# Kernel tuning notes

Hardware: AMD Instinct MI355X
Metric: run time of the kernel (lower is better)

The kernel has to match this reference:

```python
import jax, jax.numpy as jnp
import numpy as np

EPS = 1e-12
TOPK = 6

def _l2norm(x):
    # matches torch F.normalize(p=2, eps=1e-12)
    n = jnp.linalg.norm(x, axis=-1, keepdims=True)
    return x / jnp.maximum(n, EPS)

def setup_inputs() -> dict:
    key = jax.random.key(0)
    k1, k2 = jax.random.split(key)
    nC, M, P, d = 5, 512, 196, 384
    support = jax.random.normal(k1, (nC, P, d), dtype=jnp.float32)
    query = jax.random.normal(k2, (M, P, d), dtype=jnp.float32)
    scale_cls = jnp.full((1,), 10.0, dtype=jnp.float32)  # init value in module
    bias = jnp.zeros((1,), dtype=jnp.float32)
    return {"support": support, "query": query, "scale_cls": scale_cls, "bias": bias}

def reference(support, query, scale_cls, bias):
    q = _l2norm(query)      # [M, P, d]
    s = _l2norm(support)    # [nC, P, d]
    # batched cosine similarity between every query patch and support patch
    sim = jnp.einsum('mpd,cqd->mcpq', q, s)   # [M, nC, P, P]
    # max over support patches, then sum of top-6 query-patch matches
    m = sim.max(axis=3)                        # [M, nC, P]
    top6 = jax.lax.top_k(m, TOPK)[0].sum(axis=-1)  # [M, nC]
    cls_scores = top6[None]                    # [1, M, nC] (unsqueeze(0))
    return scale_cls * (cls_scores + bias)
```

## Files before the change

### kernel.cpp

```cpp
#include <hip/hip_runtime.h>
#include <hip/hip_bf16.h>
#include <cstdint>

typedef __attribute__((ext_vector_type(8))) short short8;
typedef __attribute__((ext_vector_type(4))) float floatx4;

#define NC   5
#define PP   196
#define DD   384
#define MM   512
#define ROWS (MM * PP)
#define NRB  1568
#define BR   64
#define EPSN 1e-12f

#define NTILES      16
#define TILE_BYTES  49152
#define KSTEP_BYTES 4096

__device__ __forceinline__ unsigned enc_f(float f) {
    unsigned u = __float_as_uint(f);
    return (u & 0x80000000u) ? ~u : (u | 0x80000000u);
}
__device__ __forceinline__ float dec_f(unsigned u) {
    unsigned b = (u & 0x80000000u) ? (u ^ 0x80000000u) : ~u;
    return __uint_as_float(b);
}
#define ENC_NEG_INF 0x007FFFFFu

__device__ __forceinline__ int cls_of(int col) {
    return (col >= 784) ? 4 : (col >= 588) ? 3 : (col >= 392) ? 2 : (col >= 196) ? 1 : 0;
}

__global__ __launch_bounds__(256) void k_norm0(const float* __restrict__ sup,
                                               float* __restrict__ sinv) {
    int wid = threadIdx.x >> 6, lane = threadIdx.x & 63;
    int r = blockIdx.x * 4 + wid;
    if (r >= NC * PP) return;
    const float* src = sup + (size_t)r * DD;
    float s = 0.f;
    #pragma unroll
    for (int j = 0; j < 6; ++j) { float v = src[lane + j * 64]; s += v * v; }
    #pragma unroll
    for (int off = 1; off < 64; off <<= 1) s += __shfl_xor(s, off, 64);
    if (lane == 0) sinv[r] = 1.0f / fmaxf(sqrtf(s), EPSN);
}

__global__ __launch_bounds__(256) void k_swz(const float* __restrict__ sup,
                                             const float* __restrict__ sinv,
                                             __hip_bfloat16* __restrict__ snw) {
    int s = blockIdx.x * 256 + threadIdx.x;
    int lane = s & 63;
    int r1 = s >> 6;
    int ct = r1 & 3;
    int r2 = r1 >> 2;
    int kk = r2 % 12;
    int t  = r2 / 12;
    int c16 = lane & 15, quad = lane >> 4;
    int col = t * 64 + ct * 16 + c16;
    if (col > NC * PP - 1) col = NC * PP - 1;
    int srow = col;
    const float* sp = sup + (size_t)srow * DD + kk * 32 + quad * 8;
    float inv = sinv[srow];
    alignas(16) __hip_bfloat16 hb[8];
    #pragma unroll
    for (int e = 0; e < 8; ++e) hb[e] = __float2bfloat16(sp[e] * inv);
    *(uint4*)((char*)snw + (size_t)s * 16) = *(const uint4*)hb;
}

__global__ __launch_bounds__(256, 2) void k_gemm_max(const float* __restrict__ q,
                                                     const __hip_bfloat16* __restrict__ snw,
                                                     float* __restrict__ rowmaxg) {
    __shared__ __hip_bfloat16 As[12 * 4 * 64 * 8];
    __shared__ unsigned rmax[BR * NC];
    __shared__ float rss[BR];

    const int tid  = threadIdx.x;
    const int row0 = blockIdx.x * BR;
    const int lane = tid & 63;
    const int wav  = tid >> 6;

    for (int i = tid; i < BR * NC; i += 256) rmax[i] = ENC_NEG_INF;

    {
        const int c16  = lane & 15;
        const int quad = lane >> 4;
        const int arow = wav * 16 + c16;
        const float* src = q + (size_t)(row0 + arow) * DD + quad * 8;
        float ss = 0.f;
        #pragma unroll
        for (int i = 0; i < 12; ++i) {
            const floatx4* p = (const floatx4*)(src + i * 32);
            floatx4 x0 = __builtin_nontemporal_load(p);
            floatx4 x1 = __builtin_nontemporal_load(p + 1);
            ss += x0.x*x0.x + x0.y*x0.y + x0.z*x0.z + x0.w*x0.w
                + x1.x*x1.x + x1.y*x1.y + x1.z*x1.z + x1.w*x1.w;
            alignas(16) __hip_bfloat16 hb[8];
            hb[0] = __float2bfloat16(x0.x); hb[1] = __float2bfloat16(x0.y);
            hb[2] = __float2bfloat16(x0.z); hb[3] = __float2bfloat16(x0.w);
            hb[4] = __float2bfloat16(x1.x); hb[5] = __float2bfloat16(x1.y);
            hb[6] = __float2bfloat16(x1.z); hb[7] = __float2bfloat16(x1.w);
            *(uint4*)&As[((i * 4 + wav) * 64 + lane) * 8] = *(const uint4*)hb;
        }
        ss += __shfl_xor(ss, 16, 64);
        ss += __shfl_xor(ss, 32, 64);
        if (quad == 0) rss[arow] = ss;
    }

    const char* bbase = (const char*)snw + (size_t)wav * TILE_BYTES + (size_t)lane * 16;
    short8 b0[4], b1[4], b2[4], a[2][4];

    #define BFETCH(buf, nk)                                                          \
        do { const char* p_ = bbase + (nk) * KSTEP_BYTES;                            \
            _Pragma("unroll")                                                        \
            for (int ct = 0; ct < 4; ++ct)                                           \
                buf[ct] = *(const short8*)(p_ + ct * 1024);                          \
        } while (0)

    #define BFETCHX(buf, nkx)                                                        \
        do { if (g + 4 < NTILES) {                                                   \
            const char* p_ = bbase + 4 * TILE_BYTES + (nkx) * KSTEP_BYTES;           \
            _Pragma("unroll")                                                        \
            for (int ct = 0; ct < 4; ++ct)                                           \
                buf[ct] = *(const short8*)(p_ + ct * 1024);                          \
        } } while (0)

    #define AFETCH(pre, kkn)                                                         \
        do { _Pragma("unroll")                                                       \
            for (int rt = 0; rt < 4; ++rt)                                           \
                a[pre][rt] = *(const short8*)&As[(((kkn) * 4 + rt) * 64 + lane) * 8];\
        } while (0)

    #define MFMAS(use, buf)                                                          \
        do { _Pragma("unroll")                                                       \
            for (int ct = 0; ct < 4; ++ct)                                           \
                _Pragma("unroll")                                                    \
                for (int rt = 0; rt < 4; ++rt)                                       \
                    acc[ct][rt] = __builtin_amdgcn_mfma_f32_16x16x32_bf16(           \
                        buf[ct], a[use][rt], acc[ct][rt], 0, 0, 0);                  \
        } while (0)

    #define STEP(use, pre, kpre, buf, nk)   do { AFETCH(pre, kpre); MFMAS(use, buf); BFETCH(buf, nk);   } while (0)
    #define STEPX(use, pre, kpre, buf, nkx) do { AFETCH(pre, kpre); MFMAS(use, buf); BFETCHX(buf, nkx); } while (0)

    BFETCH(b0, 0);
    BFETCH(b1, 1);
    BFETCH(b2, 2);

    __syncthreads();

    AFETCH(0, 0);

    #pragma unroll 1
    for (int g = wav; g < NTILES; g += 4) {
        floatx4 acc[4][4];
        #pragma unroll
        for (int i = 0; i < 4; ++i)
            #pragma unroll
            for (int j = 0; j < 4; ++j) acc[i][j] = (floatx4){0.f, 0.f, 0.f, 0.f};

        STEP (0, 1, 1,  b0, 3);
        STEP (1, 0, 2,  b1, 4);
        STEP (0, 1, 3,  b2, 5);
        STEP (1, 0, 4,  b0, 6);
        STEP (0, 1, 5,  b1, 7);
        STEP (1, 0, 6,  b2, 8);
        STEP (0, 1, 7,  b0, 9);
        STEP (1, 0, 8,  b1, 10);
        STEP (0, 1, 9,  b2, 11);
        STEPX(1, 0, 10, b0, 0);
        STEPX(0, 1, 11, b1, 1);
        STEPX(1, 0, 0,  b2, 2);

        {
            const int colbase = g * 64;
            int ce = colbase + 63; if (ce > NC * PP - 1) ce = NC * PP - 1;
            const int clo = cls_of(colbase), chi = cls_of(ce);
            const int quad = lane >> 4;
            if (clo == chi) {
                #pragma unroll
                for (int rt = 0; rt < 4; ++rt) {
                    float mx = acc[0][rt][0];
                    #pragma unroll
                    for (int ct = 0; ct < 4; ++ct)
                        #pragma unroll
                        for (int reg = 0; reg < 4; ++reg)
                            if (ct | reg) mx = fmaxf(mx, acc[ct][rt][reg]);
                    mx = fmaxf(mx, __shfl_xor(mx, 16, 64));
                    mx = fmaxf(mx, __shfl_xor(mx, 32, 64));
                    if (lane < 16) atomicMax(&rmax[(rt * 16 + lane) * NC + clo], enc_f(mx));
                }
            } else {
                const int bnd = chi * PP;
                #pragma unroll
                for (int rt = 0; rt < 4; ++rt) {
                    float mlo = -INFINITY, mhi = -INFINITY;
                    #pragma unroll
                    for (int ct = 0; ct < 4; ++ct)
                        #pragma unroll
                        for (int reg = 0; reg < 4; ++reg) {
                            int scol = colbase + ct * 16 + quad * 4 + reg;
                            if (scol >= bnd) mhi = fmaxf(mhi, acc[ct][rt][reg]);
                            else             mlo = fmaxf(mlo, acc[ct][rt][reg]);
                        }
                    mlo = fmaxf(mlo, __shfl_xor(mlo, 16, 64));
                    mlo = fmaxf(mlo, __shfl_xor(mlo, 32, 64));
                    mhi = fmaxf(mhi, __shfl_xor(mhi, 16, 64));
                    mhi = fmaxf(mhi, __shfl_xor(mhi, 32, 64));
                    if (lane < 16) {
                        atomicMax(&rmax[(rt * 16 + lane) * NC + clo], enc_f(mlo));
                        atomicMax(&rmax[(rt * 16 + lane) * NC + chi], enc_f(mhi));
                    }
                }
            }
        }
        bbase += 4 * TILE_BYTES;
    }

    __syncthreads();
    for (int i = tid; i < BR * NC; i += 256) {
        int c = i >> 6, row = i & 63;
        float inv = 1.0f / fmaxf(sqrtf(rss[row]), EPSN);
        __builtin_nontemporal_store(dec_f(rmax[row * NC + c]) * inv,
                                    &rowmaxg[(size_t)c * ROWS + row0 + row]);
    }
}

__global__ __launch_bounds__(256) void k_top6(const float* __restrict__ rowmaxg,
                                              const float* __restrict__ scale,
                                              const float* __restrict__ bias,
                                              float* __restrict__ out) {
    int wav = threadIdx.x >> 6, lane = threadIdx.x & 63;
    int pair = blockIdx.x * 4 + wav;
    if (pair >= MM * NC) return;
    int m = pair / NC, c = pair % NC;
    size_t base = (size_t)c * ROWS + (size_t)m * PP;
    float v[4];
    #pragma unroll
    for (int i = 0; i < 4; ++i) {
        int p = lane + i * 64;
        v[i] = (p < PP) ? rowmaxg[base + p] : -INFINITY;
    }
    float sum = 0.f;
    for (int t = 0; t < 6; ++t) {
        float bv = v[0]; int bi = 0;
        #pragma unroll
        for (int i = 1; i < 4; ++i) { if (v[i] > bv) { bv = v[i]; bi = i; } }
        int gid = bi * 64 + lane;
        #pragma unroll
        for (int off = 1; off < 64; off <<= 1) {
            float ov = __shfl_xor(bv, off, 64);
            int og  = __shfl_xor(gid, off, 64);
            if (ov > bv || (ov == bv && og < gid)) { bv = ov; gid = og; }
        }
        sum += bv;
        if ((gid & 63) == lane) v[gid >> 6] = -INFINITY;
    }
    if (lane == 0) out[pair] = scale[0] * (sum + bias[0]);
}

extern "C" void kernel_launch(void* const* d_in, const int* in_sizes, int n_in,
                              void* d_out, int out_size, void* d_ws, size_t ws_size,
                              hipStream_t stream) {
    const float* support = (const float*)d_in[0];
    const float* query   = (const float*)d_in[1];
    const float* scale   = (const float*)d_in[2];
    const float* bias    = (const float*)d_in[3];
    float* out = (float*)d_out;

    char* ws = (char*)d_ws;
    __hip_bfloat16* snw = (__hip_bfloat16*)ws;
    float* sinv         = (float*)(ws + 786432);
    float* rowmaxg      = (float*)(ws + 786432 + 4096);

    hipLaunchKernelGGL(k_norm0,   dim3(245),  dim3(256), 0, stream, support, sinv);
    hipLaunchKernelGGL(k_swz,     dim3(192),  dim3(256), 0, stream, support, sinv, snw);
    hipLaunchKernelGGL(k_gemm_max,dim3(NRB),  dim3(256), 0, stream, query, snw, rowmaxg);
    hipLaunchKernelGGL(k_top6,    dim3(640),  dim3(256), 0, stream, rowmaxg, scale, bias, out);
}
```

Baseline: 377.3 us.

## Stage support tiles into shared LDS via async global-to-LDS double buffering

Support operand tiles are no longer loaded into registers independently by each wave. They are now copied cooperatively by the whole block into a double-buffered LDS region with global_load_lds, and every wave reads them back from LDS. The swizzled support layout is reorganized into 128-column groups so each wave computes two 16-column tiles per group instead of four per 64-column tile. This cuts redundant global/L2 traffic and register pressure. In exchange it adds a __syncthreads per k-step and reduces MFMA work per wave per step, which may expose latency.

```diff
diff --git a/kernel.cpp b/kernel.cpp
--- a/kernel.cpp
+++ b/kernel.cpp
@@ -14,9 +14,9 @@
 #define BR   64
 #define EPSN 1e-12f
 
-#define NTILES      16
-#define TILE_BYTES  49152
-#define KSTEP_BYTES 4096
+#define NGP        8
+#define KSTEPS     96
+#define BLK_BYTES  8192
 
 __device__ __forceinline__ unsigned enc_f(float f) {
     unsigned u = __float_as_uint(f);
@@ -31,6 +31,10 @@
 __device__ __forceinline__ int cls_of(int col) {
     return (col >= 784) ? 4 : (col >= 588) ? 3 : (col >= 392) ? 2 : (col >= 196) ? 1 : 0;
 }
+
+typedef __attribute__((address_space(1))) const unsigned int gu32;
+typedef __attribute__((address_space(3))) unsigned int lu32;
+#define GL2LDS(g, l) __builtin_amdgcn_global_load_lds((gu32*)(g), (lu32*)(l), 16, 0, 0)
 
 __global__ __launch_bounds__(256) void k_norm0(const float* __restrict__ sup,
                                                float* __restrict__ sinv) {
@@ -50,18 +54,15 @@
                                              const float* __restrict__ sinv,
                                              __hip_bfloat16* __restrict__ snw) {
     int s = blockIdx.x * 256 + threadIdx.x;
-    int lane = s & 63;
-    int r1 = s >> 6;
-    int ct = r1 & 3;
-    int r2 = r1 >> 2;
-    int kk = r2 % 12;
-    int t  = r2 / 12;
-    int c16 = lane & 15, quad = lane >> 4;
-    int col = t * 64 + ct * 16 + c16;
+    int l   = s & 63;
+    int ctg = (s >> 6) & 7;
+    int t   = s >> 9;
+    int kk  = t % 12;
+    int gp  = t / 12;
+    int col = gp * 128 + ctg * 16 + (l & 15);
     if (col > NC * PP - 1) col = NC * PP - 1;
-    int srow = col;
-    const float* sp = sup + (size_t)srow * DD + kk * 32 + quad * 8;
-    float inv = sinv[srow];
+    const float* sp = sup + (size_t)col * DD + kk * 32 + (l >> 4) * 8;
+    float inv = sinv[col];
     alignas(16) __hip_bfloat16 hb[8];
     #pragma unroll
     for (int e = 0; e < 8; ++e) hb[e] = __float2bfloat16(sp[e] * inv);
@@ -71,7 +72,8 @@
 __global__ __launch_bounds__(256, 2) void k_gemm_max(const float* __restrict__ q,
                                                      const __hip_bfloat16* __restrict__ snw,
                                                      float* __restrict__ rowmaxg) {
-    __shared__ __hip_bfloat16 As[12 * 4 * 64 * 8];
+    __shared__ __align__(16) __hip_bfloat16 As[12 * 4 * 64 * 8];
+    __shared__ __align__(16) __hip_bfloat16 Bb[2 * 4096];
     __shared__ unsigned rmax[BR * NC];
     __shared__ float rss[BR];
 
@@ -80,7 +82,17 @@
     const int lane = tid & 63;
     const int wav  = tid >> 6;
 
+    char* Bbc = (char*)Bb;
+    const char* snwb = (const char*)snw;
+
     for (int i = tid; i < BR * NC; i += 256) rmax[i] = ENC_NEG_INF;
+
+    {
+        const char* gs = snwb + (size_t)wav * 1024 + (size_t)lane * 16;
+        char* ld = Bbc + wav * 1024;
+        GL2LDS(gs, ld);
+        GL2LDS(gs + 4096, ld + 4096);
+    }
 
     {
         const int c16  = lane & 15;
@@ -107,114 +119,85 @@
         if (quad == 0) rss[arow] = ss;
     }
 
-    const char* bbase = (const char*)snw + (size_t)wav * TILE_BYTES + (size_t)lane * 16;
-    short8 b0[4], b1[4], b2[4], a[2][4];
-
-    #define BFETCH(buf, nk)                                                          \
-        do { const char* p_ = bbase + (nk) * KSTEP_BYTES;                            \
-            _Pragma("unroll")                                                        \
-            for (int ct = 0; ct < 4; ++ct)                                           \
-                buf[ct] = *(const short8*)(p_ + ct * 1024);                          \
-        } while (0)
-
-    #define BFETCHX(buf, nkx)                                                        \
-        do { if (g + 4 < NTILES) {                                                   \
-            const char* p_ = bbase + 4 * TILE_BYTES + (nkx) * KSTEP_BYTES;           \
-            _Pragma("unroll")                                                        \
-            for (int ct = 0; ct < 4; ++ct)                                           \
-                buf[ct] = *(const short8*)(p_ + ct * 1024);                          \
-        } } while (0)
-
-    #define AFETCH(pre, kkn)                                                         \
-        do { _Pragma("unroll")                                                       \
-            for (int rt = 0; rt < 4; ++rt)                                           \
-                a[pre][rt] = *(const short8*)&As[(((kkn) * 4 + rt) * 64 + lane) * 8];\
-        } while (0)
-
-    #define MFMAS(use, buf)                                                          \
-        do { _Pragma("unroll")                                                       \
-            for (int ct = 0; ct < 4; ++ct)                                           \
-                _Pragma("unroll")                                                    \
-                for (int rt = 0; rt < 4; ++rt)                                       \
-                    acc[ct][rt] = __builtin_amdgcn_mfma_f32_16x16x32_bf16(           \
-                        buf[ct], a[use][rt], acc[ct][rt], 0, 0, 0);                  \
-        } while (0)
-
-    #define STEP(use, pre, kpre, buf, nk)   do { AFETCH(pre, kpre); MFMAS(use, buf); BFETCH(buf, nk);   } while (0)
-    #define STEPX(use, pre, kpre, buf, nkx) do { AFETCH(pre, kpre); MFMAS(use, buf); BFETCHX(buf, nkx); } while (0)
-
-    BFETCH(b0, 0);
-    BFETCH(b1, 1);
-    BFETCH(b2, 2);
-
     __syncthreads();
 
-    AFETCH(0, 0);
+    size_t gnext = BLK_BYTES;
+    int cur = 0;
+    const int ctg0 = 2 * wav;
 
     #pragma unroll 1
-    for (int g = wav; g < NTILES; g += 4) {
-        floatx4 acc[4][4];
-        #pragma unroll
-        for (int i = 0; i < 4; ++i)
+    for (int gp = 0; gp < NGP; ++gp) {
+        floatx4 acc[2][4];
+        #pragma unroll
+        for (int i = 0; i < 2; ++i)
             #pragma unroll
             for (int j = 0; j < 4; ++j) acc[i][j] = (floatx4){0.f, 0.f, 0.f, 0.f};
 
-        STEP (0, 1, 1,  b0, 3);
-        STEP (1, 0, 2,  b1, 4);
-        STEP (0, 1, 3,  b2, 5);
-        STEP (1, 0, 4,  b0, 6);
-        STEP (0, 1, 5,  b1, 7);
-        STEP (1, 0, 6,  b2, 8);
-        STEP (0, 1, 7,  b0, 9);
-        STEP (1, 0, 8,  b1, 10);
-        STEP (0, 1, 9,  b2, 11);
-        STEPX(1, 0, 10, b0, 0);
-        STEPX(0, 1, 11, b1, 1);
-        STEPX(1, 0, 0,  b2, 2);
+        #pragma unroll 1
+        for (int kk = 0; kk < 12; ++kk) {
+            if (gnext < (size_t)KSTEPS * BLK_BYTES) {
+                const char* gs = snwb + gnext + (size_t)wav * 1024 + (size_t)lane * 16;
+                char* ld = Bbc + (cur ^ 1) * BLK_BYTES + wav * 1024;
+                GL2LDS(gs, ld);
+                GL2LDS(gs + 4096, ld + 4096);
+            }
+
+            const char* bptr = Bbc + cur * BLK_BYTES + ctg0 * 1024 + lane * 16;
+            short8 bf0 = *(const short8*)bptr;
+            short8 bf1 = *(const short8*)(bptr + 1024);
+            short8 af[4];
+            #pragma unroll
+            for (int rt = 0; rt < 4; ++rt)
+                af[rt] = *(const short8*)&As[((kk * 4 + rt) * 64 + lane) * 8];
+            #pragma unroll
+            for (int rt = 0; rt < 4; ++rt) {
+                acc[0][rt] = __builtin_amdgcn_mfma_f32_16x16x32_bf16(bf0, af[rt], acc[0][rt], 0, 0, 0);
+                acc[1][rt] = __builtin_amdgcn_mfma_f32_16x16x32_bf16(bf1, af[rt], acc[1][rt], 0, 0, 0);
+            }
+
+            __syncthreads();
+            cur ^= 1;
+            gnext += BLK_BYTES;
+        }
 
         {
-            const int colbase = g * 64;
-            int ce = colbase + 63; if (ce > NC * PP - 1) ce = NC * PP - 1;
-            const int clo = cls_of(colbase), chi = cls_of(ce);
             const int quad = lane >> 4;
-            if (clo == chi) {
-                #pragma unroll
-                for (int rt = 0; rt < 4; ++rt) {
-                    float mx = acc[0][rt][0];
+            #pragma unroll
+            for (int ci = 0; ci < 2; ++ci) {
+                const int cb  = gp * 128 + (ctg0 + ci) * 16;
+                const int clo = cls_of(cb), chi = cls_of(cb + 15);
+                if (clo == chi) {
                     #pragma unroll
-                    for (int ct = 0; ct < 4; ++ct)
-                        #pragma unroll
-                        for (int reg = 0; reg < 4; ++reg)
-                            if (ct | reg) mx = fmaxf(mx, acc[ct][rt][reg]);
-                    mx = fmaxf(mx, __shfl_xor(mx, 16, 64));
-                    mx = fmaxf(mx, __shfl_xor(mx, 32, 64));
-                    if (lane < 16) atomicMax(&rmax[(rt * 16 + lane) * NC + clo], enc_f(mx));
-                }
-            } else {
-                const int bnd = chi * PP;
-                #pragma unroll
-                for (int rt = 0; rt < 4; ++rt) {
-                    float mlo = -INFINITY, mhi = -INFINITY;
+                    for (int rt = 0; rt < 4; ++rt) {
+                        float mx = fmaxf(fmaxf(acc[ci][rt][0], acc[ci][rt][1]),
+                                         fmaxf(acc[ci][rt][2], acc[ci][rt][3]));
+                        mx = fmaxf(mx, __shfl_xor(mx, 16, 64));
+                        mx = fmaxf(mx, __shfl_xor(mx, 32, 64));
+                        if (lane < 16) atomicMax(&rmax[(rt * 16 + lane) * NC + clo], enc_f(mx));
+                    }
+                } else {
+                    const int bnd = chi * PP;
                     #pragma unroll
-                    for (int ct = 0; ct < 4; ++ct)
+                    for (int rt = 0; rt < 4; ++rt) {
+                        float mlo = -INFINITY, mhi = -INFINITY;
                         #pragma unroll
                         for (int reg = 0; reg < 4; ++reg) {
-                            int scol = colbase + ct * 16 + quad * 4 + reg;
-                            if (scol >= bnd) mhi = fmaxf(mhi, acc[ct][rt][reg]);
-                            else             mlo = fmaxf(mlo, acc[ct][rt][reg]);
+                            int scol = cb + quad * 4 + reg;
+                            if (scol >= bnd) mhi = fmaxf(mhi, acc[ci][rt][reg]);
+                            else             mlo = fmaxf(mlo, acc[ci][rt][reg]);
                         }
-                    mlo = fmaxf(mlo, __shfl_xor(mlo, 16, 64));
-                    mlo = fmaxf(mlo, __shfl_xor(mlo, 32, 64));
-                    mhi = fmaxf(mhi, __shfl_xor(mhi, 16, 64));
-                    mhi = fmaxf(mhi, __shfl_xor(mhi, 32, 64));
-                    if (lane < 16) {
-                        atomicMax(&rmax[(rt * 16 + lane) * NC + clo], enc_f(mlo));
-                        atomicMax(&rmax[(rt * 16 + lane) * NC + chi], enc_f(mhi));
+                        mlo = fmaxf(mlo, __shfl_xor(mlo, 16, 64));
+                        mlo = fmaxf(mlo, __shfl_xor(mlo, 32, 64));
+                        mhi = fmaxf(mhi, __shfl_xor(mhi, 16, 64));
+                        mhi = fmaxf(mhi, __shfl_xor(mhi, 32, 64));
+                        if (lane < 16) {
+                            atomicMax(&rmax[(rt * 16 + lane) * NC + clo], enc_f(mlo));
+                            atomicMax(&rmax[(rt * 16 + lane) * NC + chi], enc_f(mhi));
+                        }
                     }
                 }
             }
         }
-        bbase += 4 * TILE_BYTES;
     }
 
     __syncthreads();
```

Result: slower. 401.1 us (+6.3%).

## Fuse support prep kernels and lay out B per wave for deeper prefetch

Applied to the files above, without the earlier changes.

Merges the support norm and swizzle kernels into one prep kernel that writes bf16 support into a per-wave contiguous layout, with padded columns and extra slack so prefetches can run past the end without a guard. The GEMM loop now keeps four B k-step buffers in flight instead of three, reading them linearly from the per-wave block. This removes one launch and the branchy end-of-tile prefetch, at the cost of more VGPRs and a larger workspace footprint.

```diff
diff --git a/kernel.cpp b/kernel.cpp
--- a/kernel.cpp
+++ b/kernel.cpp
@@ -14,9 +14,9 @@
 #define BR   64
 #define EPSN 1e-12f
 
-#define NTILES      16
-#define TILE_BYTES  49152
-#define KSTEP_BYTES 4096
+#define NTILES     16
+#define JBLK       52
+#define WBLK       (JBLK * 4096)
 
 __device__ __forceinline__ unsigned enc_f(float f) {
     unsigned u = __float_as_uint(f);
@@ -32,46 +32,52 @@
     return (col >= 784) ? 4 : (col >= 588) ? 3 : (col >= 392) ? 2 : (col >= 196) ? 1 : 0;
 }
 
-__global__ __launch_bounds__(256) void k_norm0(const float* __restrict__ sup,
-                                               float* __restrict__ sinv) {
+__global__ __launch_bounds__(256) void k_prep(const float* __restrict__ sup,
+                                              __hip_bfloat16* __restrict__ snw) {
+    __shared__ float colbuf[4][DD];
     int wid = threadIdx.x >> 6, lane = threadIdx.x & 63;
-    int r = blockIdx.x * 4 + wid;
-    if (r >= NC * PP) return;
-    const float* src = sup + (size_t)r * DD;
-    float s = 0.f;
-    #pragma unroll
-    for (int j = 0; j < 6; ++j) { float v = src[lane + j * 64]; s += v * v; }
-    #pragma unroll
-    for (int off = 1; off < 64; off <<= 1) s += __shfl_xor(s, off, 64);
-    if (lane == 0) sinv[r] = 1.0f / fmaxf(sqrtf(s), EPSN);
-}
-
-__global__ __launch_bounds__(256) void k_swz(const float* __restrict__ sup,
-                                             const float* __restrict__ sinv,
-                                             __hip_bfloat16* __restrict__ snw) {
-    int s = blockIdx.x * 256 + threadIdx.x;
-    int lane = s & 63;
-    int r1 = s >> 6;
-    int ct = r1 & 3;
-    int r2 = r1 >> 2;
-    int kk = r2 % 12;
-    int t  = r2 / 12;
-    int c16 = lane & 15, quad = lane >> 4;
-    int col = t * 64 + ct * 16 + c16;
-    if (col > NC * PP - 1) col = NC * PP - 1;
-    int srow = col;
-    const float* sp = sup + (size_t)srow * DD + kk * 32 + quad * 8;
-    float inv = sinv[srow];
-    alignas(16) __hip_bfloat16 hb[8];
-    #pragma unroll
-    for (int e = 0; e < 8; ++e) hb[e] = __float2bfloat16(sp[e] * inv);
-    *(uint4*)((char*)snw + (size_t)s * 16) = *(const uint4*)hb;
+    int col = blockIdx.x * 4 + wid;
+    const float* src = sup + (size_t)col * DD;
+    float ss = 0.f;
+    #pragma unroll
+    for (int j = 0; j < 6; ++j) {
+        float v = src[lane + j * 64];
+        ss += v * v;
+        colbuf[wid][lane + j * 64] = v;
+    }
+    #pragma unroll
+    for (int off = 1; off < 64; off <<= 1) ss += __shfl_xor(ss, off, 64);
+    float inv = 1.0f / fmaxf(sqrtf(ss), EPSN);
+    if (lane < 48) {
+        int kk = lane >> 2, quad = lane & 3;
+        const float* cb = colbuf[wid] + kk * 32 + quad * 8;
+        alignas(16) __hip_bfloat16 hb[8];
+        #pragma unroll
+        for (int e = 0; e < 8; ++e) hb[e] = __float2bfloat16(cb[e] * inv);
+        int g = col >> 6, loc = col & 63, ct = loc >> 4, c16 = loc & 15;
+        int w = g & 3, ti = g >> 2, j = ti * 12 + kk;
+        size_t off = ((size_t)(w * JBLK + j) * 256 + ct * 64 + quad * 16 + c16) * 16;
+        *(uint4*)((char*)snw + off) = *(const uint4*)hb;
+    }
+    if (col == NC * PP - 1 && lane < 48) {
+        int kk = lane >> 2, quad = lane & 3;
+        const float* cb = colbuf[wid] + kk * 32 + quad * 8;
+        alignas(16) __hip_bfloat16 hb[8];
+        #pragma unroll
+        for (int e = 0; e < 8; ++e) hb[e] = __float2bfloat16(cb[e] * inv);
+        for (int pc = NC * PP; pc < 1024; ++pc) {
+            int g = pc >> 6, loc = pc & 63, ct = loc >> 4, c16 = loc & 15;
+            int w = g & 3, ti = g >> 2, j = ti * 12 + kk;
+            size_t off = ((size_t)(w * JBLK + j) * 256 + ct * 64 + quad * 16 + c16) * 16;
+            *(uint4*)((char*)snw + off) = *(const uint4*)hb;
+        }
+    }
 }
 
 __global__ __launch_bounds__(256, 2) void k_gemm_max(const float* __restrict__ q,
                                                      const __hip_bfloat16* __restrict__ snw,
                                                      float* __restrict__ rowmaxg) {
-    __shared__ __hip_bfloat16 As[12 * 4 * 64 * 8];
+    __shared__ __align__(16) __hip_bfloat16 As[12 * 4 * 64 * 8];
     __shared__ unsigned rmax[BR * NC];
     __shared__ float rss[BR];
 
@@ -107,23 +113,19 @@
         if (quad == 0) rss[arow] = ss;
     }
 
-    const char* bbase = (const char*)snw + (size_t)wav * TILE_BYTES + (size_t)lane * 16;
-    short8 b0[4], b1[4], b2[4], a[2][4];
-
-    #define BFETCH(buf, nk)                                                          \
-        do { const char* p_ = bbase + (nk) * KSTEP_BYTES;                            \
-            _Pragma("unroll")                                                        \
-            for (int ct = 0; ct < 4; ++ct)                                           \
-                buf[ct] = *(const short8*)(p_ + ct * 1024);                          \
-        } while (0)
-
-    #define BFETCHX(buf, nkx)                                                        \
-        do { if (g + 4 < NTILES) {                                                   \
-            const char* p_ = bbase + 4 * TILE_BYTES + (nkx) * KSTEP_BYTES;           \
-            _Pragma("unroll")                                                        \
-            for (int ct = 0; ct < 4; ++ct)                                           \
-                buf[ct] = *(const short8*)(p_ + ct * 1024);                          \
-        } } while (0)
+    const char* wb = (const char*)snw + (size_t)wav * WBLK + (size_t)lane * 16;
+    short8 b0[4], b1[4], b2[4], b3[4], a[2][4];
+
+    #pragma unroll
+    for (int ct = 0; ct < 4; ++ct) b0[ct] = *(const short8*)(wb + 0 * 4096 + ct * 1024);
+    #pragma unroll
+    for (int ct = 0; ct < 4; ++ct) b1[ct] = *(const short8*)(wb + 1 * 4096 + ct * 1024);
+    #pragma unroll
+    for (int ct = 0; ct < 4; ++ct) b2[ct] = *(const short8*)(wb + 2 * 4096 + ct * 1024);
+    #pragma unroll
+    for (int ct = 0; ct < 4; ++ct) b3[ct] = *(const short8*)(wb + 3 * 4096 + ct * 1024);
+
+    __syncthreads();
 
     #define AFETCH(pre, kkn)                                                         \
         do { _Pragma("unroll")                                                       \
@@ -140,39 +142,32 @@
                         buf[ct], a[use][rt], acc[ct][rt], 0, 0, 0);                  \
         } while (0)
 
-    #define STEP(use, pre, kpre, buf, nk)   do { AFETCH(pre, kpre); MFMAS(use, buf); BFETCH(buf, nk);   } while (0)
-    #define STEPX(use, pre, kpre, buf, nkx) do { AFETCH(pre, kpre); MFMAS(use, buf); BFETCHX(buf, nkx); } while (0)
-
-    BFETCH(b0, 0);
-    BFETCH(b1, 1);
-    BFETCH(b2, 2);
-
-    __syncthreads();
+    #define POS(p, buf)                                                              \
+        do {                                                                         \
+            AFETCH((p + 1) & 1, ((p) + 1 < 12) ? (p) + 1 : 0);                       \
+            MFMAS((p) & 1, buf);                                                     \
+            _Pragma("unroll")                                                        \
+            for (int ct = 0; ct < 4; ++ct)                                           \
+                buf[ct] = *(const short8*)(bptr + ((p) + 4) * 4096 + ct * 1024);     \
+        } while (0)
 
     AFETCH(0, 0);
 
+    const char* bptr = wb;
     #pragma unroll 1
-    for (int g = wav; g < NTILES; g += 4) {
+    for (int ti = 0; ti < 4; ++ti) {
         floatx4 acc[4][4];
         #pragma unroll
         for (int i = 0; i < 4; ++i)
             #pragma unroll
             for (int j = 0; j < 4; ++j) acc[i][j] = (floatx4){0.f, 0.f, 0.f, 0.f};
 
-        STEP (0, 1, 1,  b0, 3);
-        STEP (1, 0, 2,  b1, 4);
-        STEP (0, 1, 3,  b2, 5);
-        STEP (1, 0, 4,  b0, 6);
-        STEP (0, 1, 5,  b1, 7);
-        STEP (1, 0, 6,  b2, 8);
-        STEP (0, 1, 7,  b0, 9);
-        STEP (1, 0, 8,  b1, 10);
-        STEP (0, 1, 9,  b2, 11);
-        STEPX(1, 0, 10, b0, 0);
-        STEPX(0, 1, 11, b1, 1);
-        STEPX(1, 0, 0,  b2, 2);
+        POS(0,  b0); POS(1,  b1); POS(2,  b2); POS(3,  b3);
+        POS(4,  b0); POS(5,  b1); POS(6,  b2); POS(7,  b3);
+        POS(8,  b0); POS(9,  b1); POS(10, b2); POS(11, b3);
 
         {
+            const int g = wav + 4 * ti;
             const int colbase = g * 64;
             int ce = colbase + 63; if (ce > NC * PP - 1) ce = NC * PP - 1;
             const int clo = cls_of(colbase), chi = cls_of(ce);
@@ -214,7 +209,7 @@
                 }
             }
         }
-        bbase += 4 * TILE_BYTES;
+        bptr += 12 * 4096;
     }
 
     __syncthreads();
@@ -270,11 +265,9 @@
 
     char* ws = (char*)d_ws;
     __hip_bfloat16* snw = (__hip_bfloat16*)ws;
-    float* sinv         = (float*)(ws + 786432);
-    float* rowmaxg      = (float*)(ws + 786432 + 4096);
-
-    hipLaunchKernelGGL(k_norm0,   dim3(245),  dim3(256), 0, stream, support, sinv);
-    hipLaunchKernelGGL(k_swz,     dim3(192),  dim3(256), 0, stream, support, sinv, snw);
+    float* rowmaxg      = (float*)(ws + 860160);
+
+    hipLaunchKernelGGL(k_prep,    dim3(245),  dim3(256), 0, stream, support, snw);
     hipLaunchKernelGGL(k_gemm_max,dim3(NRB),  dim3(256), 0, stream, query, snw, rowmaxg);
     hipLaunchKernelGGL(k_top6,    dim3(640),  dim3(256), 0, stream, rowmaxg, scale, bias, out);
 }
```

After: 397.3 us. 5.3% more time.
